# Kernel optimization log

Measured on AMD Instinct MI355X. Metric: run time of the kernel, lower is better.

The kernel has to match this reference:

```python
import jax, jax.numpy as jnp
import numpy as np

H = 50  # hidden_size

def setup_inputs() -> dict:
    key = jax.random.key(0)
    ks = jax.random.split(key, 7)
    B, T = 2048, 1024
    s = 1.0 / np.sqrt(H)  # PyTorch default init scale
    return {
        "x": jax.random.normal(ks[0], (B, T, 1), dtype=jnp.float32),
        "W_ih": jax.random.uniform(ks[1], (4 * H, 1), jnp.float32, -s, s),
        "W_hh": jax.random.uniform(ks[2], (4 * H, H), jnp.float32, -s, s),
        "b_ih": jax.random.uniform(ks[3], (4 * H,), jnp.float32, -s, s),
        "b_hh": jax.random.uniform(ks[4], (4 * H,), jnp.float32, -s, s),
        "W_lin": jax.random.uniform(ks[5], (1, H), jnp.float32, -s, s),
        "b_lin": jax.random.uniform(ks[6], (1,), jnp.float32, -s, s),
    }

def reference(x, W_ih, W_hh, b_ih, b_hh, W_lin, b_lin):
    B, T, _ = x.shape
    # Precompute input contribution to gates for all timesteps: [T, B, 4H]
    gx = jnp.einsum('bti,gi->tbg', x, W_ih) + (b_ih + b_hh)

    def step(carry, gx_t):
        h, c = carry
        gates = gx_t + h @ W_hh.T               # [B, 4H]
        i, f, g, o = jnp.split(gates, 4, axis=-1)  # PyTorch gate order i,f,g,o
        i = jax.nn.sigmoid(i)
        f = jax.nn.sigmoid(f)
        g = jnp.tanh(g)
        o = jax.nn.sigmoid(o)
        c = f * c + i * g
        h = o * jnp.tanh(c)
        return (h, c), None

    h0 = jnp.zeros((B, H), x.dtype)
    c0 = jnp.zeros((B, H), x.dtype)
    (h_last, _), _ = jax.lax.scan(step, (h0, c0), gx)
    # Linear head on last timestep's hidden state -> [B, 1]
    return h_last @ W_lin.T + b_lin
```

## Files before the change

### kernel.cpp

```cpp
#include <hip/hip_runtime.h>


#define H     50
#define TT    1024
#define BATCH 2048
#define BW    8
#define NTHR  448
#define KP    80

typedef float    f32x4 __attribute__((ext_vector_type(4)));
typedef _Float16 f16x8 __attribute__((ext_vector_type(8)));

__global__ __launch_bounds__(NTHR, 1) void lstm_kernel(
    const float* __restrict__ x,
    const float* __restrict__ W_ih,
    const float* __restrict__ W_hh,
    const float* __restrict__ b_ih,
    const float* __restrict__ b_hh,
    const float* __restrict__ W_lin,
    const float* __restrict__ b_lin,
    float* __restrict__ out)
{
    __shared__ _Float16 hb[2][BW][KP];
    __shared__ float    XT[TT + 2][BW];
    __shared__ float    redH[H][BW];

    const int tid  = threadIdx.x;
    const int wave = tid >> 6;
    const int lane = tid & 63;
    const int L15  = lane & 15;
    const int kq   = lane >> 4;
    const int bl   = L15 & 7;
    const int b0   = blockIdx.x * BW;

    const int t0 = 2 * wave;

    const float LOG2E  = 1.4426950408889634f;
    const float LOG2E2 = 2.8853900817779268f;

    f16x8 A[2][2];
    #pragma unroll
    for (int tt = 0; tt < 2; ++tt) {
        const int m  = (t0 + tt) * 16 + L15;
        const int jm = m >> 2, gm = m & 3;
        const bool v = (jm < H);
        const float s = (gm == 2) ? LOG2E2 : -LOG2E;
        #pragma unroll
        for (int kf = 0; kf < 2; ++kf) {
            f16x8 vv;
            #pragma unroll
            for (int e = 0; e < 8; ++e) {
                const int k = kf * 32 + kq * 8 + e;
                _Float16 val = (_Float16)0.f;
                if (v && k < H) val = (_Float16)(s * W_hh[(gm * H + jm) * H + k]);
                vv[e] = val;
            }
            A[tt][kf] = vv;
        }
    }

    const int  j  = 8 * wave + ((L15 >> 3) << 2) + kq;
    const bool jv = (j < H);
    const float wlin = jv ? W_lin[j] : 0.f;
    float zw[4], zb[4];
    #pragma unroll
    for (int r = 0; r < 4; ++r) {
        const float s = (r == 2) ? LOG2E2 : -LOG2E;
        zw[r] = jv ? s * W_ih[r * H + j] : 0.f;
        zb[r] = jv ? s * (b_ih[r * H + j] + b_hh[r * H + j]) : 0.f;
    }

    for (int i = tid; i < 2 * BW * KP; i += NTHR)
        ((_Float16*)hb)[i] = (_Float16)0.f;
    for (int i = tid; i < TT * BW; i += NTHR) {
        const int bb = i >> 10, t = i & 1023;
        XT[t][bb] = x[(size_t)(b0 + bb) * TT + t];
    }
    if (tid < 2 * BW) ((float*)&XT[TT][0])[tid] = 0.f;

    float c2 = 0.f;
    float hlast = 0.f;
    __syncthreads();

    float xt_cur = XT[0][bl];
    const bool lo = (L15 < 8);

    #pragma unroll 1
    for (int tbase = 0; tbase < TT; tbase += 2) {
        #pragma unroll
        for (int half = 0; half < 2; ++half) {
            const int t = tbase + half;
            const _Float16* hp = &hb[half][bl][0];
            _Float16*       np = &hb[half ^ 1][bl][0];

            const f16x8 B0 = *(const f16x8*)(hp + kq * 8);
            const f16x8 B1 = *(const f16x8*)(hp + 32 + kq * 8);

            f32x4 zc;
            #pragma unroll
            for (int r = 0; r < 4; ++r)
                zc[r] = __builtin_fmaf(zw[r], xt_cur, zb[r]);

            f32x4 a0 = __builtin_amdgcn_mfma_f32_16x16x32_f16(A[0][0], B0, zc, 0, 0, 0);
            f32x4 a1 = __builtin_amdgcn_mfma_f32_16x16x32_f16(A[1][0], B0, zc, 0, 0, 0);
            a0 = __builtin_amdgcn_mfma_f32_16x16x32_f16(A[0][1], B1, a0, 0, 0, 0);
            a1 = __builtin_amdgcn_mfma_f32_16x16x32_f16(A[1][1], B1, a1, 0, 0, 0);

            const float xt_nxt = XT[t + 1][bl];

            const float gi = lo ? a0[0] : a1[0];
            const float gf = lo ? a0[1] : a1[1];
            const float gg = lo ? a0[2] : a1[2];
            const float go = lo ? a0[3] : a1[3];

            const float Ei = __builtin_amdgcn_exp2f(gi);
            const float Ef = __builtin_amdgcn_exp2f(gf);
            const float Eg = __builtin_amdgcn_exp2f(gg);
            const float Eo = __builtin_amdgcn_exp2f(go);
            const float P  = (1.0f + Ei) * (1.0f + Eg);
            const float Q2 = __builtin_fmaf(LOG2E2, Ef, LOG2E2);
            const float num = __builtin_fmaf(c2, P, (Eg - 1.0f) * Q2);
            const float PQ  = P * (1.0f + Ef);
            c2 = num * __builtin_amdgcn_rcpf(PQ);
            const float ca = fminf(c2, 80.0f);
            const float Ec = __builtin_amdgcn_exp2f(ca);
            const float h  = (Ec - 1.0f) *
                __builtin_amdgcn_rcpf((1.0f + Eo) * (1.0f + Ec));
            hlast = h;

            np[j] = (_Float16)h;
            __syncthreads();
            xt_cur = xt_nxt;
        }
    }

    if (jv) redH[j][bl] = wlin * hlast;
    __syncthreads();
    if (tid < BW) {
        float s = b_lin[0];
        #pragma unroll 10
        for (int jj = 0; jj < H; ++jj) s += redH[jj][tid];
        out[b0 + tid] = s;
    }
}

extern "C" void kernel_launch(void* const* d_in, const int* in_sizes, int n_in,
                              void* d_out, int out_size, void* d_ws, size_t ws_size,
                              hipStream_t stream) {
    const float* x     = (const float*)d_in[0];
    const float* W_ih  = (const float*)d_in[1];
    const float* W_hh  = (const float*)d_in[2];
    const float* b_ih  = (const float*)d_in[3];
    const float* b_hh  = (const float*)d_in[4];
    const float* W_lin = (const float*)d_in[5];
    const float* b_lin = (const float*)d_in[6];
    float* out = (float*)d_out;

    dim3 grid(BATCH / BW);
    dim3 block(NTHR);
    lstm_kernel<<<grid, block, 0, stream>>>(x, W_ih, W_hh, b_ih, b_hh,
                                            W_lin, b_lin, out);
}
```

Measured before the change: 333.3 us.

## Interleave two independent batch groups per block to hide recurrence latency

Each block still processes 8 sequences, but they are now split into two groups of 4 whose LSTM steps alternate, ping-ponging between separate h buffers. The B-operand load for one group is issued before the other group's compute, so LDS latency and the MFMA-to-transcendental dependency chain can overlap with the other group's work. This doubles the number of barriers per timestep. Each MFMA now carries only 4 useful batch columns (replicated across lanes), so half the lanes do redundant work and only some of them write back.

Result: slower. 538.3 us (+61.5%).

```diff
diff --git a/kernel.cpp b/kernel.cpp
--- a/kernel.cpp
+++ b/kernel.cpp
@@ -4,7 +4,8 @@
 #define H     50
 #define TT    1024
 #define BATCH 2048
-#define BW    8
+#define BW    4
+#define NG    2
 #define NTHR  448
 #define KP    80
 
@@ -21,17 +22,18 @@
     const float* __restrict__ b_lin,
     float* __restrict__ out)
 {
-    __shared__ _Float16 hb[2][BW][KP];
-    __shared__ float    XT[TT + 2][BW];
-    __shared__ float    redH[H][BW];
+    __shared__ _Float16 hb[NG][2][BW][KP];
+    __shared__ float    XT[TT + 2][NG * BW];
+    __shared__ float    redH[H][NG * BW];
 
     const int tid  = threadIdx.x;
     const int wave = tid >> 6;
     const int lane = tid & 63;
     const int L15  = lane & 15;
     const int kq   = lane >> 4;
-    const int bl   = L15 & 7;
-    const int b0   = blockIdx.x * BW;
+    const int bl   = L15 & 3;
+    const int rep  = L15 >> 2;
+    const int b0   = blockIdx.x * (NG * BW);
 
     const int t0 = 2 * wave;
 
@@ -59,8 +61,9 @@
         }
     }
 
-    const int  j  = 8 * wave + ((L15 >> 3) << 2) + kq;
+    const int  j  = 8 * wave + 4 * (rep & 1) + kq;
     const bool jv = (j < H);
+    const bool wr = (L15 < 8);
     const float wlin = jv ? W_lin[j] : 0.f;
     float zw[4], zb[4];
     #pragma unroll
@@ -70,73 +73,121 @@
         zb[r] = jv ? s * (b_ih[r * H + j] + b_hh[r * H + j]) : 0.f;
     }
 
-    for (int i = tid; i < 2 * BW * KP; i += NTHR)
+    for (int i = tid; i < NG * 2 * BW * KP; i += NTHR)
         ((_Float16*)hb)[i] = (_Float16)0.f;
-    for (int i = tid; i < TT * BW; i += NTHR) {
+    for (int i = tid; i < TT * NG * BW; i += NTHR) {
         const int bb = i >> 10, t = i & 1023;
         XT[t][bb] = x[(size_t)(b0 + bb) * TT + t];
     }
-    if (tid < 2 * BW) ((float*)&XT[TT][0])[tid] = 0.f;
-
-    float c2 = 0.f;
-    float hlast = 0.f;
+    if (tid < 2 * NG * BW) ((float*)&XT[TT][0])[tid] = 0.f;
+
+    float c2A = 0.f, c2B = 0.f;
+    float hAf = 0.f, hBf = 0.f;
     __syncthreads();
 
-    float xt_cur = XT[0][bl];
-    const bool lo = (L15 < 8);
+    f16x8 fA0 = {};
+    f16x8 fA1 = {};
+    float xA = XT[0][bl];
+    float xB = XT[0][BW + bl];
+    const bool lo = ((rep & 1) == 0);
 
     #pragma unroll 1
     for (int tbase = 0; tbase < TT; tbase += 2) {
         #pragma unroll
-        for (int half = 0; half < 2; ++half) {
-            const int t = tbase + half;
-            const _Float16* hp = &hb[half][bl][0];
-            _Float16*       np = &hb[half ^ 1][bl][0];
-
-            const f16x8 B0 = *(const f16x8*)(hp + kq * 8);
-            const f16x8 B1 = *(const f16x8*)(hp + 32 + kq * 8);
-
-            f32x4 zc;
-            #pragma unroll
-            for (int r = 0; r < 4; ++r)
-                zc[r] = __builtin_fmaf(zw[r], xt_cur, zb[r]);
-
-            f32x4 a0 = __builtin_amdgcn_mfma_f32_16x16x32_f16(A[0][0], B0, zc, 0, 0, 0);
-            f32x4 a1 = __builtin_amdgcn_mfma_f32_16x16x32_f16(A[1][0], B0, zc, 0, 0, 0);
-            a0 = __builtin_amdgcn_mfma_f32_16x16x32_f16(A[0][1], B1, a0, 0, 0, 0);
-            a1 = __builtin_amdgcn_mfma_f32_16x16x32_f16(A[1][1], B1, a1, 0, 0, 0);
-
-            const float xt_nxt = XT[t + 1][bl];
-
-            const float gi = lo ? a0[0] : a1[0];
-            const float gf = lo ? a0[1] : a1[1];
-            const float gg = lo ? a0[2] : a1[2];
-            const float go = lo ? a0[3] : a1[3];
-
-            const float Ei = __builtin_amdgcn_exp2f(gi);
-            const float Ef = __builtin_amdgcn_exp2f(gf);
-            const float Eg = __builtin_amdgcn_exp2f(gg);
-            const float Eo = __builtin_amdgcn_exp2f(go);
-            const float P  = (1.0f + Ei) * (1.0f + Eg);
-            const float Q2 = __builtin_fmaf(LOG2E2, Ef, LOG2E2);
-            const float num = __builtin_fmaf(c2, P, (Eg - 1.0f) * Q2);
-            const float PQ  = P * (1.0f + Ef);
-            c2 = num * __builtin_amdgcn_rcpf(PQ);
-            const float ca = fminf(c2, 80.0f);
-            const float Ec = __builtin_amdgcn_exp2f(ca);
-            const float h  = (Ec - 1.0f) *
-                __builtin_amdgcn_rcpf((1.0f + Eo) * (1.0f + Ec));
-            hlast = h;
-
-            np[j] = (_Float16)h;
+        for (int p = 0; p < 2; ++p) {
+            const int t = tbase + p;
+
+            const _Float16* hpB = &hb[1][p][bl][0];
+            const f16x8 fB0 = *(const f16x8*)(hpB + kq * 8);
+            const f16x8 fB1 = *(const f16x8*)(hpB + 32 + kq * 8);
+
+            {
+                f32x4 zc;
+                #pragma unroll
+                for (int r = 0; r < 4; ++r)
+                    zc[r] = __builtin_fmaf(zw[r], xA, zb[r]);
+
+                f32x4 a0 = __builtin_amdgcn_mfma_f32_16x16x32_f16(A[0][0], fA0, zc, 0, 0, 0);
+                f32x4 a1 = __builtin_amdgcn_mfma_f32_16x16x32_f16(A[1][0], fA0, zc, 0, 0, 0);
+                a0 = __builtin_amdgcn_mfma_f32_16x16x32_f16(A[0][1], fA1, a0, 0, 0, 0);
+                a1 = __builtin_amdgcn_mfma_f32_16x16x32_f16(A[1][1], fA1, a1, 0, 0, 0);
+
+                xA = XT[t + 1][bl];
+
+                const float gi = lo ? a0[0] : a1[0];
+                const float gf = lo ? a0[1] : a1[1];
+                const float gg = lo ? a0[2] : a1[2];
+                const float go = lo ? a0[3] : a1[3];
+
+                const float Ei = __builtin_amdgcn_exp2f(gi);
+                const float Ef = __builtin_amdgcn_exp2f(gf);
+                const float Eg = __builtin_amdgcn_exp2f(gg);
+                const float Eo = __builtin_amdgcn_exp2f(go);
+                const float P  = (1.0f + Ei) * (1.0f + Eg);
+                const float Q2 = __builtin_fmaf(LOG2E2, Ef, LOG2E2);
+                const float num = __builtin_fmaf(c2A, P, (Eg - 1.0f) * Q2);
+                const float PQ  = P * (1.0f + Ef);
+                c2A = num * __builtin_amdgcn_rcpf(PQ);
+                const float ca = fminf(c2A, 80.0f);
+                const float Ec = __builtin_amdgcn_exp2f(ca);
+                hAf = (Ec - 1.0f) *
+                    __builtin_amdgcn_rcpf((1.0f + Eo) * (1.0f + Ec));
+
+                if (wr) (&hb[0][p ^ 1][bl][0])[j] = (_Float16)hAf;
+            }
             __syncthreads();
-            xt_cur = xt_nxt;
+
+            const _Float16* hpA = &hb[0][p ^ 1][bl][0];
+            const f16x8 nA0 = *(const f16x8*)(hpA + kq * 8);
+            const f16x8 nA1 = *(const f16x8*)(hpA + 32 + kq * 8);
+
+            {
+                f32x4 zc;
+                #pragma unroll
+                for (int r = 0; r < 4; ++r)
+                    zc[r] = __builtin_fmaf(zw[r], xB, zb[r]);
+
+                f32x4 a0 = __builtin_amdgcn_mfma_f32_16x16x32_f16(A[0][0], fB0, zc, 0, 0, 0);
+                f32x4 a1 = __builtin_amdgcn_mfma_f32_16x16x32_f16(A[1][0], fB0, zc, 0, 0, 0);
+                a0 = __builtin_amdgcn_mfma_f32_16x16x32_f16(A[0][1], fB1, a0, 0, 0, 0);
+                a1 = __builtin_amdgcn_mfma_f32_16x16x32_f16(A[1][1], fB1, a1, 0, 0, 0);
+
+                xB = XT[t + 1][BW + bl];
+
+                const float gi = lo ? a0[0] : a1[0];
+                const float gf = lo ? a0[1] : a1[1];
+                const float gg = lo ? a0[2] : a1[2];
+                const float go = lo ? a0[3] : a1[3];
+
+                const float Ei = __builtin_amdgcn_exp2f(gi);
+                const float Ef = __builtin_amdgcn_exp2f(gf);
+                const float Eg = __builtin_amdgcn_exp2f(gg);
+                const float Eo = __builtin_amdgcn_exp2f(go);
+                const float P  = (1.0f + Ei) * (1.0f + Eg);
+                const float Q2 = __builtin_fmaf(LOG2E2, Ef, LOG2E2);
+                const float num = __builtin_fmaf(c2B, P, (Eg - 1.0f) * Q2);
+                const float PQ  = P * (1.0f + Ef);
+                c2B = num * __builtin_amdgcn_rcpf(PQ);
+                const float ca = fminf(c2B, 80.0f);
+                const float Ec = __builtin_amdgcn_exp2f(ca);
+                hBf = (Ec - 1.0f) *
+                    __builtin_amdgcn_rcpf((1.0f + Eo) * (1.0f + Ec));
+
+                if (wr) (&hb[1][p ^ 1][bl][0])[j] = (_Float16)hBf;
+            }
+            __syncthreads();
+
+            fA0 = nA0;
+            fA1 = nA1;
         }
     }
 
-    if (jv) redH[j][bl] = wlin * hlast;
+    if (jv && wr) {
+        redH[j][bl]      = wlin * hAf;
+        redH[j][BW + bl] = wlin * hBf;
+    }
     __syncthreads();
-    if (tid < BW) {
+    if (tid < NG * BW) {
         float s = b_lin[0];
         #pragma unroll 10
         for (int jj = 0; jj < H; ++jj) s += redH[jj][tid];
@@ -156,7 +207,7 @@
     const float* b_lin = (const float*)d_in[6];
     float* out = (float*)d_out;
 
-    dim3 grid(BATCH / BW);
+    dim3 grid(BATCH / (NG * BW));
     dim3 block(NTHR);
     lstm_kernel<<<grid, block, 0, stream>>>(x, W_ih, W_hh, b_ih, b_hh,
                                             W_lin, b_lin, out);
```
